# Kernel tuning notes

Hardware: AMD Instinct MI355X
Metric: run time of the kernel (lower is better)

Reference implementation:

```python
import jax, jax.numpy as jnp
import numpy as np


def _conv1x1(x, W, b):
    # x: [B, Cin, H, W]; W: [Cout, Cin]; b: [Cout] -- 1x1 conv == channel matmul
    return jnp.einsum('oc,bchw->bohw', W, x) + b[None, :, None, None]


def setup_inputs() -> dict:
    key = jax.random.key(0)
    ks = jax.random.split(key, 9)
    B, C, H, W = 8, 64, 64, 64
    x = jax.random.normal(ks[0], (B, C, H, W), dtype=jnp.float32)
    y = jax.random.normal(ks[1], (B, C, H, W), dtype=jnp.float32)
    scale = 1.0 / np.sqrt(C)
    Wq = jax.random.normal(ks[2], (C, C), dtype=jnp.float32) * scale
    bq = jax.random.normal(ks[3], (C,), dtype=jnp.float32) * 0.01
    Wk = jax.random.normal(ks[4], (C, C), dtype=jnp.float32) * scale
    bk = jax.random.normal(ks[5], (C,), dtype=jnp.float32) * 0.01
    Wv = jax.random.normal(ks[6], (C, C), dtype=jnp.float32) * scale
    bv = jax.random.normal(ks[7], (C,), dtype=jnp.float32) * 0.01
    # torch inits gamma to 0; use small nonzero value so output/grads are non-trivial
    gamma = jax.random.normal(ks[8], (1,), dtype=jnp.float32) * 0.1
    return {"x": x, "y": y, "Wq": Wq, "bq": bq, "Wk": Wk, "bk": bk,
            "Wv": Wv, "bv": bv, "gamma": gamma}


def reference(x, y, Wq, bq, Wk, bk, Wv, bv, gamma):
    B, C, H, W = x.shape
    N = H * W
    q = _conv1x1(x, Wq, bq)  # [B, C, H, W]
    k = _conv1x1(y, Wk, bk)
    v = _conv1x1(y, Wv, bv)
    # Faithful to torch: raw .view(B, -1, C) memory reinterpretation (NOT a transpose)
    qf = q.reshape(B, N, C)   # reinterprets [B,C,H,W] buffer as [B, N, C]
    kf = k.reshape(B, C, N)
    vf = v.reshape(B, C, N)
    att = jnp.einsum('bnc,bcm->bnm', qf, kf)          # [B, N, N], unscaled
    att = jax.nn.softmax(att, axis=-1)
    out = jnp.einsum('bcj,bij->bci', vf, att)         # bmm(v, att^T) -> [B, C, N]
    out = out.reshape(B, C, H, W)
    return gamma[0] * out + x
```

## Files before the change

kernel.cpp:

```cpp
#include <hip/hip_runtime.h>
#include <math.h>

#define Bb 8
#define Cc 64
#define Nn 4096
#define LOG2E 1.4426950408889634f
#define DEFER_TH 8.0f

typedef __attribute__((ext_vector_type(8))) short bf16x8;
typedef __attribute__((ext_vector_type(4))) float f32x4;
typedef __attribute__((ext_vector_type(4))) int   i32x4;

#define MFMA(a,b,c) __builtin_amdgcn_mfma_f32_16x16x32_bf16((a),(b),(c),0,0,0)

#if __has_builtin(__builtin_amdgcn_exp2f)
#define EXP2F(x) __builtin_amdgcn_exp2f(x)
#else
#define EXP2F(x) exp2f(x)
#endif

__device__ __forceinline__ unsigned short f2bf(float f){
    unsigned uu = __float_as_uint(f);
    return (unsigned short)((uu + 0x7FFFu + ((uu>>16)&1u)) >> 16);
}
__device__ __forceinline__ float bfres(float f, unsigned short h){
    return f - __uint_as_float(((unsigned)h)<<16);
}
__device__ __forceinline__ int swzaddr(int row, int slot){
    int h = (row ^ (row>>3)) & 7;
    return row*128 + (((slot ^ h)&7)<<4);
}

__global__ __launch_bounds__(256) void precompute_q(
    const float* __restrict__ x, const float* __restrict__ Wq,
    const float* __restrict__ bq, unsigned short* __restrict__ wsq)
{
    __shared__ __align__(16) unsigned char XHI[16384];
    __shared__ __align__(16) unsigned char XLO[16384];
    const int tid = threadIdx.x;
    const int l   = tid & 63;
    const int w   = tid >> 6;
    const int l15 = l & 15;
    const int u   = l >> 4;
    const int b   = blockIdx.x & 7;
    const int pt  = blockIdx.x >> 3;
    const int p0  = pt*128;

    bf16x8 whiA[2], wloA[2];
    #pragma unroll
    for (int kc=0; kc<2; ++kc){
        const float* wr = Wq + (16*w + l15)*64 + kc*32 + u*8;
        const float4 f0 = *(const float4*)(wr);
        const float4 f1 = *(const float4*)(wr + 4);
        const float vv[8] = {f0.x,f0.y,f0.z,f0.w,f1.x,f1.y,f1.z,f1.w};
        bf16x8 hi, lo;
        #pragma unroll
        for (int i=0;i<8;++i){
            const unsigned short h = f2bf(vv[i]);
            hi[i] = (short)h;
            lo[i] = (short)f2bf(bfres(vv[i], h));
        }
        whiA[kc]=hi; wloA[kc]=lo;
    }
    {
        const int cx0 = (tid & 31)*2;
        const int pq  = (tid >> 5)*16;
        const float* xr0 = x + ((size_t)b*64 + cx0)*4096 + p0 + pq;
        const float* xr1 = xr0 + 4096;
        #pragma unroll
        for (int q4=0; q4<4; ++q4){
            const float4 a = *(const float4*)(xr0 + q4*4);
            const float4 c = *(const float4*)(xr1 + q4*4);
            const float av[4]={a.x,a.y,a.z,a.w}, cv[4]={c.x,c.y,c.z,c.w};
            #pragma unroll
            for (int k=0;k<4;++k){
                const int p = pq + q4*4 + k;
                const unsigned short h0=f2bf(av[k]), h1=f2bf(cv[k]);
                const unsigned short l0=f2bf(bfres(av[k],h0));
                const unsigned short l1=f2bf(bfres(cv[k],h1));
                const int ad = swzaddr(p, cx0>>3) + (cx0&7)*2;
                *(unsigned int*)(XHI + ad) = (unsigned)h0 | ((unsigned)h1<<16);
                *(unsigned int*)(XLO + ad) = (unsigned)l0 | ((unsigned)l1<<16);
            }
        }
    }
    __syncthreads();

    f32x4 D[8];
    #pragma unroll
    for (int nb=0;nb<8;++nb) D[nb]=(f32x4){0.f,0.f,0.f,0.f};
    #pragma unroll
    for (int nb=0;nb<8;++nb){
        #pragma unroll
        for (int kc=0;kc<2;++kc){
            const int ad = swzaddr(16*nb + l15, kc*4 + u);
            const bf16x8 xh = *(const bf16x8*)(XHI + ad);
            const bf16x8 xl = *(const bf16x8*)(XLO + ad);
            D[nb] = MFMA(whiA[kc], xh, D[nb]);
            D[nb] = MFMA(whiA[kc], xl, D[nb]);
            D[nb] = MFMA(wloA[kc], xh, D[nb]);
        }
    }
    float bq4[4];
    #pragma unroll
    for (int r=0;r<4;++r) bq4[r] = bq[16*w + u*4 + r];
    #pragma unroll
    for (int nb=0;nb<8;++nb){
        #pragma unroll
        for (int r=0;r<4;++r){
            const int c = 16*w + u*4 + r;
            const int p = p0 + 16*nb + l15;
            wsq[((size_t)b*64 + c)*4096 + p] = f2bf(D[nb][r] + bq4[r]);
        }
    }
}

__global__ __launch_bounds__(256,2) void fused_attn2(
    const float* __restrict__ x, const float* __restrict__ y,
    const float* __restrict__ Wk, const unsigned short* __restrict__ wsq,
    const float* __restrict__ Wv, const float* __restrict__ bv,
    const float* __restrict__ gammap, float* __restrict__ out)
{
    __shared__ __align__(16) unsigned char QW [8192];
    __shared__ __align__(16) unsigned char PT [8192];
    __shared__ __align__(16) unsigned char WKT[8192];
    __shared__ __align__(16) unsigned char YN [2][8192];
    __shared__ __align__(16) unsigned char YT [2][8192];

    const int tid = threadIdx.x;
    const int l   = tid & 63;
    const int w   = tid >> 6;
    const int l15 = l & 15;
    const int u   = l >> 4;
    const int b   = blockIdx.x & 7;
    const int blk = blockIdx.x >> 3;
    const int p0  = blk*64;

    const float* __restrict__ yb = y + (size_t)b*Cc*Nn;

    const int sci = tid >> 2;
    const int sj0 = (tid & 3) * 16;

    float4 pf0, pf1, pf2, pf3;
    {
        const float* yr = yb + (size_t)sci*Nn + sj0;
        pf0 = *(const float4*)(yr);
        pf1 = *(const float4*)(yr + 4);
        pf2 = *(const float4*)(yr + 8);
        pf3 = *(const float4*)(yr + 12);
    }

    {
        const int c   = tid >> 2;
        const int ci0 = (tid & 3)*16;
        const float* wr = Wk + c*64 + ci0;
        #pragma unroll
        for (int q4=0; q4<4; ++q4){
            const float4 f = *(const float4*)(wr + q4*4);
            const float fv[4] = {f.x,f.y,f.z,f.w};
            #pragma unroll
            for (int k=0;k<4;++k){
                const int ci = ci0 + q4*4 + k;
                *(unsigned short*)(WKT + swzaddr(ci, c>>3) + (c&7)*2) = f2bf(fv[k]);
            }
        }
    }
    bf16x8 qA[2];
    {
        const unsigned short* qchan = wsq + ((size_t)b*64 + blk)*4096;
        #pragma unroll
        for (int kc=0;kc<2;++kc)
            qA[kc] = *(const bf16x8*)(qchan + 64*(16*w + l15) + kc*32 + u*8);
    }
    __syncthreads();

    {
        f32x4 D2[4];
        #pragma unroll
        for (int nb=0;nb<4;++nb){
            f32x4 d = (f32x4){0.f,0.f,0.f,0.f};
            d = MFMA(qA[0], *(const bf16x8*)(WKT + swzaddr(16*nb + l15, u)),     d);
            d = MFMA(qA[1], *(const bf16x8*)(WKT + swzaddr(16*nb + l15, 4 + u)), d);
            D2[nb] = d;
        }
        #pragma unroll
        for (int nb=0;nb<4;++nb){
            #pragma unroll
            for (int r=0;r<4;++r){
                const int t  = 16*w + u*4 + r;
                const int ci = 16*nb + l15;
                *(unsigned short*)(QW + swzaddr(t, 2*nb + (l15>>3)) + (l15&7)*2)
                    = f2bf(D2[nb][r] * LOG2E);
            }
        }
    }
    bf16x8 qwA[2];
    qwA[0] = *(const bf16x8*)(QW + swzaddr(16*w + l15, u));
    qwA[1] = *(const bf16x8*)(QW + swzaddr(16*w + l15, 4 + u));

    int rd[4][2];
    #pragma unroll
    for (int nb=0;nb<4;++nb){
        rd[nb][0] = swzaddr(16*nb + l15, u);
        rd[nb][1] = swzaddr(16*nb + l15, 4 + u);
    }
    const int paA0 = swzaddr(16*w + l15, u);
    const int paA1 = swzaddr(16*w + l15, 4 + u);
    int pw[4][4];
    #pragma unroll
    for (int r=0;r<4;++r)
        #pragma unroll
        for (int nb=0;nb<4;++nb)
            pw[r][nb] = swzaddr(16*w + u*4 + r, 2*nb + (l15>>3)) + (l15&7)*2;

    auto stage_write = [&](float4 a0, float4 a1, float4 a2, float4 a3, int buf){
        const float v[16] = {a0.x,a0.y,a0.z,a0.w, a1.x,a1.y,a1.z,a1.w,
                             a2.x,a2.y,a2.z,a2.w, a3.x,a3.y,a3.z,a3.w};
        unsigned short e[16];
        #pragma unroll
        for (int k=0;k<16;++k) e[k] = f2bf(v[k]);
        i32x4 pk0, pk1;
        pk0.x = (int)((unsigned)e[0]  | ((unsigned)e[1]<<16));
        pk0.y = (int)((unsigned)e[2]  | ((unsigned)e[3]<<16));
        pk0.z = (int)((unsigned)e[4]  | ((unsigned)e[5]<<16));
        pk0.w = (int)((unsigned)e[6]  | ((unsigned)e[7]<<16));
        pk1.x = (int)((unsigned)e[8]  | ((unsigned)e[9]<<16));
        pk1.y = (int)((unsigned)e[10] | ((unsigned)e[11]<<16));
        pk1.z = (int)((unsigned)e[12] | ((unsigned)e[13]<<16));
        pk1.w = (int)((unsigned)e[14] | ((unsigned)e[15]<<16));
        *(i32x4*)(YN[buf] + swzaddr(sci, (sj0>>3)))     = pk0;
        *(i32x4*)(YN[buf] + swzaddr(sci, (sj0>>3) + 1)) = pk1;
        #pragma unroll
        for (int k=0;k<16;++k)
            *(unsigned short*)(YT[buf] + swzaddr(sj0 + k, sci>>3) + (sci&7)*2) = e[k];
    };

    stage_write(pf0, pf1, pf2, pf3, 0);
    __syncthreads();

    f32x4 PY[4];
    #pragma unroll
    for (int nb=0;nb<4;++nb) PY[nb] = (f32x4){0.f,0.f,0.f,0.f};
    float m4[4], l4[4];
    #pragma unroll
    for (int r=0;r<4;++r){ m4[r] = -1.0e30f; l4[r] = 0.f; }

    for (int jt = 0; jt < 64; ++jt){
        const int cur = jt & 1;
        float4 n0,n1,n2,n3;
        if (jt < 63){
            const float* yr = yb + (size_t)sci*Nn + (jt+1)*64 + sj0;
            n0 = *(const float4*)(yr);
            n1 = *(const float4*)(yr + 4);
            n2 = *(const float4*)(yr + 8);
            n3 = *(const float4*)(yr + 12);
        }
        f32x4 S[4];
        #pragma unroll
        for (int nb=0;nb<4;++nb){
            f32x4 s = (f32x4){0.f,0.f,0.f,0.f};
            s = MFMA(qwA[0], *(const bf16x8*)(YT[cur] + rd[nb][0]), s);
            s = MFMA(qwA[1], *(const bf16x8*)(YT[cur] + rd[nb][1]), s);
            S[nb] = s;
        }
        float pm[4];
        #pragma unroll
        for (int r=0;r<4;++r)
            pm[r] = fmaxf(fmaxf(S[0][r],S[1][r]), fmaxf(S[2][r],S[3][r]));
        #pragma unroll
        for (int st=1; st<16; st<<=1){
            #pragma unroll
            for (int r=0;r<4;++r) pm[r] = fmaxf(pm[r], __shfl_xor(pm[r], st));
        }
        bool need = false;
        #pragma unroll
        for (int r=0;r<4;++r) need = need || (pm[r] > m4[r] + DEFER_TH);
        if (__ballot(need)) {
            #pragma unroll
            for (int r=0;r<4;++r){
                const float mn = fmaxf(m4[r], pm[r]);
                const float sc = EXP2F(m4[r] - mn);
                m4[r] = mn;
                l4[r] *= sc;
                #pragma unroll
                for (int nb=0;nb<4;++nb) PY[nb][r] *= sc;
            }
        }
        float rs[4] = {0.f,0.f,0.f,0.f};
        #pragma unroll
        for (int nb=0;nb<4;++nb){
            #pragma unroll
            for (int r=0;r<4;++r){
                const float e = EXP2F(S[nb][r] - m4[r]);
                S[nb][r] = e;
                rs[r] += e;
            }
        }
        #pragma unroll
        for (int st=1; st<16; st<<=1){
            #pragma unroll
            for (int r=0;r<4;++r) rs[r] += __shfl_xor(rs[r], st);
        }
        #pragma unroll
        for (int r=0;r<4;++r) l4[r] += rs[r];

        #pragma unroll
        for (int r=0;r<4;++r)
            #pragma unroll
            for (int nb=0;nb<4;++nb)
                *(unsigned short*)(PT + pw[r][nb]) = f2bf(S[nb][r]);
        {
            const bf16x8 pa0 = *(const bf16x8*)(PT + paA0);
            const bf16x8 pa1 = *(const bf16x8*)(PT + paA1);
            #pragma unroll
            for (int nb=0;nb<4;++nb){
                f32x4 acc = PY[nb];
                acc = MFMA(pa0, *(const bf16x8*)(YN[cur] + rd[nb][0]), acc);
                acc = MFMA(pa1, *(const bf16x8*)(YN[cur] + rd[nb][1]), acc);
                PY[nb] = acc;
            }
        }
        if (jt < 63) stage_write(n0, n1, n2, n3, cur ^ 1);
        __syncthreads();
    }

    float inv[4];
    #pragma unroll
    for (int r=0;r<4;++r) inv[r] = 1.0f / l4[r];
    #pragma unroll
    for (int r=0;r<4;++r)
        #pragma unroll
        for (int nb=0;nb<4;++nb)
            *(unsigned short*)(PT + pw[r][nb]) = f2bf(PY[nb][r] * inv[r]);
    __syncthreads();

    {
        bf16x8 wvA[2];
        #pragma unroll
        for (int kc=0;kc<2;++kc){
            const float* wr = Wv + (16*w + l15)*64 + kc*32 + u*8;
            const float4 f0 = *(const float4*)(wr);
            const float4 f1 = *(const float4*)(wr + 4);
            const float vv[8] = {f0.x,f0.y,f0.z,f0.w,f1.x,f1.y,f1.z,f1.w};
            bf16x8 t;
            #pragma unroll
            for (int i=0;i<8;++i) t[i] = (short)f2bf(vv[i]);
            wvA[kc] = t;
        }
        f32x4 O[4];
        #pragma unroll
        for (int nb=0;nb<4;++nb){
            f32x4 o = (f32x4){0.f,0.f,0.f,0.f};
            o = MFMA(wvA[0], *(const bf16x8*)(PT + rd[nb][0]), o);
            o = MFMA(wvA[1], *(const bf16x8*)(PT + rd[nb][1]), o);
            O[nb] = o;
        }
        const float g = gammap[0];
        #pragma unroll
        for (int r=0;r<4;++r){
            const int cout = 16*w + u*4 + r;
            const float bvc = bv[cout];
            #pragma unroll
            for (int nb=0;nb<4;++nb){
                const int t = 16*nb + l15;
                const size_t oi = ((size_t)b*64 + cout)*4096 + p0 + t;
                out[oi] = g*(O[nb][r] + bvc) + x[oi];
            }
        }
    }
}

extern "C" void kernel_launch(void* const* d_in, const int* in_sizes, int n_in,
                              void* d_out, int out_size, void* d_ws, size_t ws_size,
                              hipStream_t stream) {
    const float* x  = (const float*)d_in[0];
    const float* y  = (const float*)d_in[1];
    const float* Wq = (const float*)d_in[2];
    const float* bq = (const float*)d_in[3];
    const float* Wk = (const float*)d_in[4];
    const float* Wv = (const float*)d_in[6];
    const float* bv = (const float*)d_in[7];
    const float* g  = (const float*)d_in[8];
    float* outp = (float*)d_out;
    unsigned short* wsq = (unsigned short*)d_ws;

    hipLaunchKernelGGL(precompute_q, dim3(256), dim3(256), 0, stream,
                       x, Wq, bq, wsq);
    hipLaunchKernelGGL(fused_attn2, dim3(512), dim3(256), 0, stream,
                       x, y, Wk, wsq, Wv, bv, g, outp);
}
```

Baseline: 221.2 us.

## Rewrite attention kernel with 32x32 MFMA tiles and register-resident P

The fused attention kernel is rewritten around 32x32x16 bf16 MFMA tiles, with 128 queries per block and 256 blocks instead of 512 blocks of 64 queries. Q·Wk folding, the softmax probabilities and the final Wv projection are kept in registers through lane shuffles and packing, so the QW, PT and WKT shared-memory staging buffers are gone. The y tile staging now writes the transposed copy with vectorized 16-byte stores, and bf16 conversion uses a cheaper round-half-up pack. The precompute_q x staging is also restructured into per-thread column loads with vector LDS writes. The trade-offs are higher register pressure (launch bound lowered to 1 block per SM), half as many blocks to fill the GPU, and slightly different rounding.

```diff
diff --git a/kernel.cpp b/kernel.cpp
--- a/kernel.cpp
+++ b/kernel.cpp
@@ -1,22 +1,22 @@
 #include <hip/hip_runtime.h>
 #include <math.h>
 
-#define Bb 8
-#define Cc 64
-#define Nn 4096
 #define LOG2E 1.4426950408889634f
 #define DEFER_TH 8.0f
 
-typedef __attribute__((ext_vector_type(8))) short bf16x8;
-typedef __attribute__((ext_vector_type(4))) float f32x4;
-typedef __attribute__((ext_vector_type(4))) int   i32x4;
-
-#define MFMA(a,b,c) __builtin_amdgcn_mfma_f32_16x16x32_bf16((a),(b),(c),0,0,0)
+typedef __attribute__((ext_vector_type(8)))  short bf16x8;
+typedef __attribute__((ext_vector_type(4)))  short bf16x4;
+typedef __attribute__((ext_vector_type(4)))  float f32x4;
+typedef __attribute__((ext_vector_type(16))) float f32x16;
+typedef __attribute__((ext_vector_type(4)))  int   i32x4;
+
+#define MFMA16(a,b,c) __builtin_amdgcn_mfma_f32_16x16x32_bf16((a),(b),(c),0,0,0)
+#define MFMA32(a,b,c) __builtin_amdgcn_mfma_f32_32x32x16_bf16((a),(b),(c),0,0,0)
 
 #if __has_builtin(__builtin_amdgcn_exp2f)
-#define EXP2F(x) __builtin_amdgcn_exp2f(x)
+#define EXP2F(v) __builtin_amdgcn_exp2f(v)
 #else
-#define EXP2F(x) exp2f(x)
+#define EXP2F(v) exp2f(v)
 #endif
 
 __device__ __forceinline__ unsigned short f2bf(float f){
@@ -26,10 +26,19 @@
 __device__ __forceinline__ float bfres(float f, unsigned short h){
     return f - __uint_as_float(((unsigned)h)<<16);
 }
-__device__ __forceinline__ int swzaddr(int row, int slot){
-    int h = (row ^ (row>>3)) & 7;
-    return row*128 + (((slot ^ h)&7)<<4);
-}
+__device__ __forceinline__ unsigned packrn(float a, float b){
+    unsigned ua = (__float_as_uint(a) + 0x8000u) >> 16;
+    unsigned ub = (__float_as_uint(b) + 0x8000u) & 0xFFFF0000u;
+    return ua | ub;
+}
+__device__ __forceinline__ unsigned packne(float a, float b){
+    return (unsigned)f2bf(a) | ((unsigned)f2bf(b) << 16);
+}
+__device__ __forceinline__ int lds_rc(int row, int slot){
+    int h = (row ^ (row >> 3)) & 7;
+    return (row << 7) + (((slot ^ h) & 7) << 4);
+}
+union U4 { unsigned u[4]; bf16x8 v; i32x4 i; };
 
 __global__ __launch_bounds__(256) void precompute_q(
     const float* __restrict__ x, const float* __restrict__ Wq,
@@ -38,13 +47,12 @@
     __shared__ __align__(16) unsigned char XHI[16384];
     __shared__ __align__(16) unsigned char XLO[16384];
     const int tid = threadIdx.x;
-    const int l   = tid & 63;
+    const int l15 = tid & 15;
+    const int u   = (tid & 63) >> 4;
     const int w   = tid >> 6;
-    const int l15 = l & 15;
-    const int u   = l >> 4;
     const int b   = blockIdx.x & 7;
     const int pt  = blockIdx.x >> 3;
-    const int p0  = pt*128;
+    const int p0  = pt * 128;
 
     bf16x8 whiA[2], wloA[2];
     #pragma unroll
@@ -63,42 +71,43 @@
         whiA[kc]=hi; wloA[kc]=lo;
     }
     {
-        const int cx0 = (tid & 31)*2;
-        const int pq  = (tid >> 5)*16;
-        const float* xr0 = x + ((size_t)b*64 + cx0)*4096 + p0 + pq;
-        const float* xr1 = xr0 + 4096;
-        #pragma unroll
-        for (int q4=0; q4<4; ++q4){
-            const float4 a = *(const float4*)(xr0 + q4*4);
-            const float4 c = *(const float4*)(xr1 + q4*4);
-            const float av[4]={a.x,a.y,a.z,a.w}, cv[4]={c.x,c.y,c.z,c.w};
-            #pragma unroll
-            for (int k=0;k<4;++k){
-                const int p = pq + q4*4 + k;
-                const unsigned short h0=f2bf(av[k]), h1=f2bf(cv[k]);
-                const unsigned short l0=f2bf(bfres(av[k],h0));
-                const unsigned short l1=f2bf(bfres(cv[k],h1));
-                const int ad = swzaddr(p, cx0>>3) + (cx0&7)*2;
-                *(unsigned int*)(XHI + ad) = (unsigned)h0 | ((unsigned)h1<<16);
-                *(unsigned int*)(XLO + ad) = (unsigned)l0 | ((unsigned)l1<<16);
-            }
+        const int p  = tid & 127;
+        const int hf = tid >> 7;
+        const float* xr = x + ((size_t)(b*64 + hf*32))*4096 + p0 + p;
+        float v[32];
+        #pragma unroll
+        for (int k2=0;k2<32;++k2) v[k2] = xr[(size_t)k2*4096];
+        unsigned hiw[16], low[16];
+        #pragma unroll
+        for (int q2=0;q2<16;++q2){
+            const unsigned short h0 = f2bf(v[2*q2]),  h1 = f2bf(v[2*q2+1]);
+            const unsigned short r0 = f2bf(bfres(v[2*q2],h0)), r1 = f2bf(bfres(v[2*q2+1],h1));
+            hiw[q2] = (unsigned)h0 | ((unsigned)h1<<16);
+            low[q2] = (unsigned)r0 | ((unsigned)r1<<16);
+        }
+        #pragma unroll
+        for (int s=0;s<4;++s){
+            i32x4 a = {(int)hiw[4*s],(int)hiw[4*s+1],(int)hiw[4*s+2],(int)hiw[4*s+3]};
+            i32x4 c2= {(int)low[4*s],(int)low[4*s+1],(int)low[4*s+2],(int)low[4*s+3]};
+            *(i32x4*)(XHI + lds_rc(p, hf*4 + s)) = a;
+            *(i32x4*)(XLO + lds_rc(p, hf*4 + s)) = c2;
         }
     }
     __syncthreads();
 
     f32x4 D[8];
     #pragma unroll
-    for (int nb=0;nb<8;++nb) D[nb]=(f32x4){0.f,0.f,0.f,0.f};
+    for (int nb=0;nb<8;++nb) D[nb] = (f32x4){0.f,0.f,0.f,0.f};
     #pragma unroll
     for (int nb=0;nb<8;++nb){
         #pragma unroll
         for (int kc=0;kc<2;++kc){
-            const int ad = swzaddr(16*nb + l15, kc*4 + u);
+            const int ad = lds_rc(16*nb + l15, 4*kc + u);
             const bf16x8 xh = *(const bf16x8*)(XHI + ad);
             const bf16x8 xl = *(const bf16x8*)(XLO + ad);
-            D[nb] = MFMA(whiA[kc], xh, D[nb]);
-            D[nb] = MFMA(whiA[kc], xl, D[nb]);
-            D[nb] = MFMA(wloA[kc], xh, D[nb]);
+            D[nb] = MFMA16(whiA[kc], xh, D[nb]);
+            D[nb] = MFMA16(whiA[kc], xl, D[nb]);
+            D[nb] = MFMA16(wloA[kc], xh, D[nb]);
         }
     }
     float bq4[4];
@@ -107,265 +116,261 @@
     #pragma unroll
     for (int nb=0;nb<8;++nb){
         #pragma unroll
-        for (int r=0;r<4;++r){
-            const int c = 16*w + u*4 + r;
-            const int p = p0 + 16*nb + l15;
-            wsq[((size_t)b*64 + c)*4096 + p] = f2bf(D[nb][r] + bq4[r]);
-        }
-    }
-}
-
-__global__ __launch_bounds__(256,2) void fused_attn2(
+        for (int r=0;r<4;++r)
+            wsq[((size_t)b*64 + 16*w + u*4 + r)*4096 + p0 + 16*nb + l15]
+                = f2bf(D[nb][r] + bq4[r]);
+    }
+}
+
+__global__ __launch_bounds__(256, 1) void fused_attn3(
     const float* __restrict__ x, const float* __restrict__ y,
     const float* __restrict__ Wk, const unsigned short* __restrict__ wsq,
     const float* __restrict__ Wv, const float* __restrict__ bv,
     const float* __restrict__ gammap, float* __restrict__ out)
 {
-    __shared__ __align__(16) unsigned char QW [8192];
-    __shared__ __align__(16) unsigned char PT [8192];
-    __shared__ __align__(16) unsigned char WKT[8192];
-    __shared__ __align__(16) unsigned char YN [2][8192];
-    __shared__ __align__(16) unsigned char YT [2][8192];
+    __shared__ __align__(16) unsigned char YN[2][8192];
+    __shared__ __align__(16) unsigned char YT[2][8192];
 
     const int tid = threadIdx.x;
     const int l   = tid & 63;
     const int w   = tid >> 6;
-    const int l15 = l & 15;
-    const int u   = l >> 4;
+    const int l31 = l & 31;
+    const int g   = l >> 5;
     const int b   = blockIdx.x & 7;
-    const int blk = blockIdx.x >> 3;
-    const int p0  = blk*64;
-
-    const float* __restrict__ yb = y + (size_t)b*Cc*Nn;
-
-    const int sci = tid >> 2;
-    const int sj0 = (tid & 3) * 16;
-
-    float4 pf0, pf1, pf2, pf3;
+    const int pb  = blockIdx.x >> 3;
+    const int n0  = pb * 128;
+
+    const float* __restrict__ yb = y + (size_t)b*64*4096;
+
+    f32x16 QC0, QC1;
+    #pragma unroll
+    for (int i=0;i<16;++i){ QC0[i]=0.f; QC1[i]=0.f; }
     {
-        const float* yr = yb + (size_t)sci*Nn + sj0;
-        pf0 = *(const float4*)(yr);
-        pf1 = *(const float4*)(yr + 4);
-        pf2 = *(const float4*)(yr + 8);
-        pf3 = *(const float4*)(yr + 12);
-    }
-
+        const int ch  = (pb*2) + (w >> 1);
+        const unsigned short* qrow = wsq + ((size_t)b*64 + ch)*4096 + ((w&1)*32 + l31)*64;
+        #pragma unroll
+        for (int kc=0;kc<4;++kc){
+            const bf16x8 qb = *(const bf16x8*)(qrow + 16*kc + g*8);
+            #pragma unroll
+            for (int rowb=0;rowb<2;++rowb){
+                bf16x8 wa;
+                #pragma unroll
+                for (int i=0;i<8;++i)
+                    wa[i] = (short)f2bf(Wk[(16*kc + g*8 + i)*64 + 32*rowb + l31]);
+                if (rowb==0) QC0 = MFMA32(wa, qb, QC0);
+                else         QC1 = MFMA32(wa, qb, QC1);
+            }
+        }
+    }
+    bf16x8 qwB[4];
     {
-        const int c   = tid >> 2;
-        const int ci0 = (tid & 3)*16;
-        const float* wr = Wk + c*64 + ci0;
-        #pragma unroll
-        for (int q4=0; q4<4; ++q4){
-            const float4 f = *(const float4*)(wr + q4*4);
-            const float fv[4] = {f.x,f.y,f.z,f.w};
-            #pragma unroll
-            for (int k=0;k<4;++k){
-                const int ci = ci0 + q4*4 + k;
-                *(unsigned short*)(WKT + swzaddr(ci, c>>3) + (c&7)*2) = f2bf(fv[k]);
-            }
-        }
-    }
-    bf16x8 qA[2];
+        unsigned qp[2][8], qq[2][8];
+        #pragma unroll
+        for (int m=0;m<8;++m){
+            qp[0][m] = packne(QC0[2*m]*LOG2E, QC0[2*m+1]*LOG2E);
+            qp[1][m] = packne(QC1[2*m]*LOG2E, QC1[2*m+1]*LOG2E);
+        }
+        #pragma unroll
+        for (int rb=0;rb<2;++rb)
+            #pragma unroll
+            for (int m=0;m<8;++m) qq[rb][m] = __shfl_xor((int)qp[rb][m], 32);
+        #pragma unroll
+        for (int kc=0;kc<4;++kc){
+            const int rb = kc>>1, h = kc&1;
+            U4 uu;
+            if (g==0){ uu.u[0]=qp[rb][4*h+0]; uu.u[1]=qp[rb][4*h+1];
+                       uu.u[2]=qq[rb][4*h+0]; uu.u[3]=qq[rb][4*h+1]; }
+            else     { uu.u[0]=qq[rb][4*h+2]; uu.u[1]=qq[rb][4*h+3];
+                       uu.u[2]=qp[rb][4*h+2]; uu.u[3]=qp[rb][4*h+3]; }
+            qwB[kc] = uu.v;
+        }
+    }
+
+    const int nci = tid >> 2, njq = tid & 3;
+    const int tj  = tid & 63, tcq = tid >> 6;
+    const int wnat0 = lds_rc(nci, njq*2),     wnat1 = lds_rc(nci, njq*2 + 1);
+    const int wtr0  = lds_rc(tj,  tcq*2),     wtr1  = lds_rc(tj,  tcq*2 + 1);
+    int rS[2][4];
+    #pragma unroll
+    for (int jb=0;jb<2;++jb)
+        #pragma unroll
+        for (int kc=0;kc<4;++kc) rS[jb][kc] = lds_rc(32*jb + l31, 2*kc + g);
+    int rPa[2][4][2];
+    #pragma unroll
+    for (int cib=0;cib<2;++cib)
+        #pragma unroll
+        for (int kcp=0;kcp<4;++kcp){
+            const int jb = kcp>>1, h = kcp&1;
+            rPa[cib][kcp][0] = lds_rc(l31 + 32*cib, 4*jb + 2*h)     + 8*g;
+            rPa[cib][kcp][1] = lds_rc(l31 + 32*cib, 4*jb + 2*h + 1) + 8*g;
+        }
+    const float* gnat = yb + (size_t)nci*4096 + njq*16;
+    const float* gtr  = yb + (size_t)(tcq*16)*4096 + tj;
+
+    f32x16 OC0, OC1;
+    #pragma unroll
+    for (int i=0;i<16;++i){ OC0[i]=0.f; OC1[i]=0.f; }
+    float m = -1.0e30f, lsum = 0.f;
+
     {
-        const unsigned short* qchan = wsq + ((size_t)b*64 + blk)*4096;
-        #pragma unroll
-        for (int kc=0;kc<2;++kc)
-            qA[kc] = *(const bf16x8*)(qchan + 64*(16*w + l15) + kc*32 + u*8);
+        float4 a0 = *(const float4*)(gnat);
+        float4 a1 = *(const float4*)(gnat + 4);
+        float4 a2 = *(const float4*)(gnat + 8);
+        float4 a3 = *(const float4*)(gnat + 12);
+        float tv[16];
+        #pragma unroll
+        for (int k2=0;k2<16;++k2) tv[k2] = gtr[(size_t)k2*4096];
+        const float nvv[16] = {a0.x,a0.y,a0.z,a0.w,a1.x,a1.y,a1.z,a1.w,
+                               a2.x,a2.y,a2.z,a2.w,a3.x,a3.y,a3.z,a3.w};
+        unsigned nk[8], tk[8];
+        #pragma unroll
+        for (int q2=0;q2<8;++q2){ nk[q2]=packrn(nvv[2*q2],nvv[2*q2+1]);
+                                  tk[q2]=packrn(tv[2*q2], tv[2*q2+1]); }
+        i32x4 w0={(int)nk[0],(int)nk[1],(int)nk[2],(int)nk[3]};
+        i32x4 w1={(int)nk[4],(int)nk[5],(int)nk[6],(int)nk[7]};
+        i32x4 w2={(int)tk[0],(int)tk[1],(int)tk[2],(int)tk[3]};
+        i32x4 w3={(int)tk[4],(int)tk[5],(int)tk[6],(int)tk[7]};
+        *(i32x4*)(YN[0] + wnat0) = w0;  *(i32x4*)(YN[0] + wnat1) = w1;
+        *(i32x4*)(YT[0] + wtr0)  = w2;  *(i32x4*)(YT[0] + wtr1)  = w3;
     }
     __syncthreads();
-
-    {
-        f32x4 D2[4];
-        #pragma unroll
-        for (int nb=0;nb<4;++nb){
-            f32x4 d = (f32x4){0.f,0.f,0.f,0.f};
-            d = MFMA(qA[0], *(const bf16x8*)(WKT + swzaddr(16*nb + l15, u)),     d);
-            d = MFMA(qA[1], *(const bf16x8*)(WKT + swzaddr(16*nb + l15, 4 + u)), d);
-            D2[nb] = d;
-        }
-        #pragma unroll
-        for (int nb=0;nb<4;++nb){
-            #pragma unroll
-            for (int r=0;r<4;++r){
-                const int t  = 16*w + u*4 + r;
-                const int ci = 16*nb + l15;
-                *(unsigned short*)(QW + swzaddr(t, 2*nb + (l15>>3)) + (l15&7)*2)
-                    = f2bf(D2[nb][r] * LOG2E);
-            }
-        }
-    }
-    bf16x8 qwA[2];
-    qwA[0] = *(const bf16x8*)(QW + swzaddr(16*w + l15, u));
-    qwA[1] = *(const bf16x8*)(QW + swzaddr(16*w + l15, 4 + u));
-
-    int rd[4][2];
-    #pragma unroll
-    for (int nb=0;nb<4;++nb){
-        rd[nb][0] = swzaddr(16*nb + l15, u);
-        rd[nb][1] = swzaddr(16*nb + l15, 4 + u);
-    }
-    const int paA0 = swzaddr(16*w + l15, u);
-    const int paA1 = swzaddr(16*w + l15, 4 + u);
-    int pw[4][4];
-    #pragma unroll
-    for (int r=0;r<4;++r)
-        #pragma unroll
-        for (int nb=0;nb<4;++nb)
-            pw[r][nb] = swzaddr(16*w + u*4 + r, 2*nb + (l15>>3)) + (l15&7)*2;
-
-    auto stage_write = [&](float4 a0, float4 a1, float4 a2, float4 a3, int buf){
-        const float v[16] = {a0.x,a0.y,a0.z,a0.w, a1.x,a1.y,a1.z,a1.w,
-                             a2.x,a2.y,a2.z,a2.w, a3.x,a3.y,a3.z,a3.w};
-        unsigned short e[16];
-        #pragma unroll
-        for (int k=0;k<16;++k) e[k] = f2bf(v[k]);
-        i32x4 pk0, pk1;
-        pk0.x = (int)((unsigned)e[0]  | ((unsigned)e[1]<<16));
-        pk0.y = (int)((unsigned)e[2]  | ((unsigned)e[3]<<16));
-        pk0.z = (int)((unsigned)e[4]  | ((unsigned)e[5]<<16));
-        pk0.w = (int)((unsigned)e[6]  | ((unsigned)e[7]<<16));
-        pk1.x = (int)((unsigned)e[8]  | ((unsigned)e[9]<<16));
-        pk1.y = (int)((unsigned)e[10] | ((unsigned)e[11]<<16));
-        pk1.z = (int)((unsigned)e[12] | ((unsigned)e[13]<<16));
-        pk1.w = (int)((unsigned)e[14] | ((unsigned)e[15]<<16));
-        *(i32x4*)(YN[buf] + swzaddr(sci, (sj0>>3)))     = pk0;
-        *(i32x4*)(YN[buf] + swzaddr(sci, (sj0>>3) + 1)) = pk1;
-        #pragma unroll
-        for (int k=0;k<16;++k)
-            *(unsigned short*)(YT[buf] + swzaddr(sj0 + k, sci>>3) + (sci&7)*2) = e[k];
-    };
-
-    stage_write(pf0, pf1, pf2, pf3, 0);
-    __syncthreads();
-
-    f32x4 PY[4];
-    #pragma unroll
-    for (int nb=0;nb<4;++nb) PY[nb] = (f32x4){0.f,0.f,0.f,0.f};
-    float m4[4], l4[4];
-    #pragma unroll
-    for (int r=0;r<4;++r){ m4[r] = -1.0e30f; l4[r] = 0.f; }
 
     for (int jt = 0; jt < 64; ++jt){
         const int cur = jt & 1;
-        float4 n0,n1,n2,n3;
-        if (jt < 63){
-            const float* yr = yb + (size_t)sci*Nn + (jt+1)*64 + sj0;
-            n0 = *(const float4*)(yr);
-            n1 = *(const float4*)(yr + 4);
-            n2 = *(const float4*)(yr + 8);
-            n3 = *(const float4*)(yr + 12);
-        }
-        f32x4 S[4];
-        #pragma unroll
-        for (int nb=0;nb<4;++nb){
-            f32x4 s = (f32x4){0.f,0.f,0.f,0.f};
-            s = MFMA(qwA[0], *(const bf16x8*)(YT[cur] + rd[nb][0]), s);
-            s = MFMA(qwA[1], *(const bf16x8*)(YT[cur] + rd[nb][1]), s);
-            S[nb] = s;
-        }
-        float pm[4];
-        #pragma unroll
-        for (int r=0;r<4;++r)
-            pm[r] = fmaxf(fmaxf(S[0][r],S[1][r]), fmaxf(S[2][r],S[3][r]));
-        #pragma unroll
-        for (int st=1; st<16; st<<=1){
-            #pragma unroll
-            for (int r=0;r<4;++r) pm[r] = fmaxf(pm[r], __shfl_xor(pm[r], st));
-        }
-        bool need = false;
-        #pragma unroll
-        for (int r=0;r<4;++r) need = need || (pm[r] > m4[r] + DEFER_TH);
-        if (__ballot(need)) {
-            #pragma unroll
-            for (int r=0;r<4;++r){
-                const float mn = fmaxf(m4[r], pm[r]);
-                const float sc = EXP2F(m4[r] - mn);
-                m4[r] = mn;
-                l4[r] *= sc;
+        const bool pf = (jt < 63);
+        float4 a0,a1,a2,a3; float tv[16];
+        if (pf){
+            const float* gn = gnat + (jt+1)*64;
+            a0 = *(const float4*)(gn);     a1 = *(const float4*)(gn + 4);
+            a2 = *(const float4*)(gn + 8); a3 = *(const float4*)(gn + 12);
+            const float* gt = gtr + (jt+1)*64;
+            #pragma unroll
+            for (int k2=0;k2<16;++k2) tv[k2] = gt[(size_t)k2*4096];
+        }
+        f32x16 SC0, SC1;
+        #pragma unroll
+        for (int i=0;i<16;++i){ SC0[i]=0.f; SC1[i]=0.f; }
+        #pragma unroll
+        for (int kc=0;kc<4;++kc){
+            SC0 = MFMA32(*(const bf16x8*)(YT[cur] + rS[0][kc]), qwB[kc], SC0);
+            SC1 = MFMA32(*(const bf16x8*)(YT[cur] + rS[1][kc]), qwB[kc], SC1);
+        }
+        float mx[16];
+        #pragma unroll
+        for (int i=0;i<16;++i) mx[i] = fmaxf(SC0[i], SC1[i]);
+        #pragma unroll
+        for (int s=8;s>=1;s>>=1)
+            #pragma unroll
+            for (int i=0;i<s;++i) mx[i] = fmaxf(mx[i], mx[i+s]);
+        float pm = fmaxf(mx[0], __shfl_xor(mx[0], 32));
+        if (__ballot(pm > m + DEFER_TH)) {
+            const float mn = fmaxf(m, pm);
+            const float sc = EXP2F(m - mn);
+            m = mn; lsum *= sc;
+            #pragma unroll
+            for (int i=0;i<16;++i){ OC0[i]*=sc; OC1[i]*=sc; }
+        }
+        float p0f[16], p1f[16];
+        #pragma unroll
+        for (int i=0;i<16;++i){ p0f[i]=EXP2F(SC0[i]-m); p1f[i]=EXP2F(SC1[i]-m); }
+        float sm[16];
+        #pragma unroll
+        for (int i=0;i<16;++i) sm[i] = p0f[i] + p1f[i];
+        #pragma unroll
+        for (int s=8;s>=1;s>>=1)
+            #pragma unroll
+            for (int i=0;i<s;++i) sm[i] += sm[i+s];
+        lsum += sm[0] + __shfl_xor(sm[0], 32);
+        unsigned pk0[8], pk1[8];
+        #pragma unroll
+        for (int q2=0;q2<8;++q2){ pk0[q2]=packrn(p0f[2*q2],p0f[2*q2+1]);
+                                  pk1[q2]=packrn(p1f[2*q2],p1f[2*q2+1]); }
+        #pragma unroll
+        for (int kcp=0;kcp<4;++kcp){
+            const int h = kcp&1;
+            U4 pb4;
+            if (kcp<2){ pb4.u[0]=pk0[4*h+0]; pb4.u[1]=pk0[4*h+1];
+                        pb4.u[2]=pk0[4*h+2]; pb4.u[3]=pk0[4*h+3]; }
+            else      { pb4.u[0]=pk1[4*h+0]; pb4.u[1]=pk1[4*h+1];
+                        pb4.u[2]=pk1[4*h+2]; pb4.u[3]=pk1[4*h+3]; }
+            {
+                bf16x4 y0 = *(const bf16x4*)(YN[cur] + rPa[0][kcp][0]);
+                bf16x4 y1 = *(const bf16x4*)(YN[cur] + rPa[0][kcp][1]);
+                bf16x8 ya; 
                 #pragma unroll
-                for (int nb=0;nb<4;++nb) PY[nb][r] *= sc;
+                for (int i=0;i<4;++i){ ya[i]=y0[i]; ya[4+i]=y1[i]; }
+                OC0 = MFMA32(ya, pb4.v, OC0);
             }
-        }
-        float rs[4] = {0.f,0.f,0.f,0.f};
-        #pragma unroll
-        for (int nb=0;nb<4;++nb){
-            #pragma unroll
-            for (int r=0;r<4;++r){
-                const float e = EXP2F(S[nb][r] - m4[r]);
-                S[nb][r] = e;
-                rs[r] += e;
+            {
+                bf16x4 y0 = *(const bf16x4*)(YN[cur] + rPa[1][kcp][0]);
+                bf16x4 y1 = *(const bf16x4*)(YN[cur] + rPa[1][kcp][1]);
+                bf16x8 ya;
+                #pragma unroll
+                for (int i=0;i<4;++i){ ya[i]=y0[i]; ya[4+i]=y1[i]; }
+                OC1 = MFMA32(ya, pb4.v, OC1);
             }
         }
-        #pragma unroll
-        for (int st=1; st<16; st<<=1){
-            #pragma unroll
-            for (int r=0;r<4;++r) rs[r] += __shfl_xor(rs[r], st);
-        }
-        #pragma unroll
-        for (int r=0;r<4;++r) l4[r] += rs[r];
-
-        #pragma unroll
-        for (int r=0;r<4;++r)
-            #pragma unroll
-            for (int nb=0;nb<4;++nb)
-                *(unsigned short*)(PT + pw[r][nb]) = f2bf(S[nb][r]);
-        {
-            const bf16x8 pa0 = *(const bf16x8*)(PT + paA0);
-            const bf16x8 pa1 = *(const bf16x8*)(PT + paA1);
-            #pragma unroll
-            for (int nb=0;nb<4;++nb){
-                f32x4 acc = PY[nb];
-                acc = MFMA(pa0, *(const bf16x8*)(YN[cur] + rd[nb][0]), acc);
-                acc = MFMA(pa1, *(const bf16x8*)(YN[cur] + rd[nb][1]), acc);
-                PY[nb] = acc;
-            }
-        }
-        if (jt < 63) stage_write(n0, n1, n2, n3, cur ^ 1);
+        if (pf){
+            const float nvv[16] = {a0.x,a0.y,a0.z,a0.w,a1.x,a1.y,a1.z,a1.w,
+                                   a2.x,a2.y,a2.z,a2.w,a3.x,a3.y,a3.z,a3.w};
+            unsigned nk[8], tk[8];
+            #pragma unroll
+            for (int q2=0;q2<8;++q2){ nk[q2]=packrn(nvv[2*q2],nvv[2*q2+1]);
+                                      tk[q2]=packrn(tv[2*q2], tv[2*q2+1]); }
+            const int nxt = cur ^ 1;
+            i32x4 w0={(int)nk[0],(int)nk[1],(int)nk[2],(int)nk[3]};
+            i32x4 w1={(int)nk[4],(int)nk[5],(int)nk[6],(int)nk[7]};
+            i32x4 w2={(int)tk[0],(int)tk[1],(int)tk[2],(int)tk[3]};
+            i32x4 w3={(int)tk[4],(int)tk[5],(int)tk[6],(int)tk[7]};
+            *(i32x4*)(YN[nxt] + wnat0) = w0;  *(i32x4*)(YN[nxt] + wnat1) = w1;
+            *(i32x4*)(YT[nxt] + wtr0)  = w2;  *(i32x4*)(YT[nxt] + wtr1)  = w3;
+        }
         __syncthreads();
     }
 
-    float inv[4];
-    #pragma unroll
-    for (int r=0;r<4;++r) inv[r] = 1.0f / l4[r];
-    #pragma unroll
-    for (int r=0;r<4;++r)
-        #pragma unroll
-        for (int nb=0;nb<4;++nb)
-            *(unsigned short*)(PT + pw[r][nb]) = f2bf(PY[nb][r] * inv[r]);
-    __syncthreads();
-
-    {
-        bf16x8 wvA[2];
-        #pragma unroll
-        for (int kc=0;kc<2;++kc){
-            const float* wr = Wv + (16*w + l15)*64 + kc*32 + u*8;
+    const float inv = 1.0f / lsum;
+    unsigned ok0[8], ok1[8];
+    #pragma unroll
+    for (int q2=0;q2<8;++q2){
+        ok0[q2] = packne(OC0[2*q2]*inv, OC0[2*q2+1]*inv);
+        ok1[q2] = packne(OC1[2*q2]*inv, OC1[2*q2+1]*inv);
+    }
+    f32x16 ZC0, ZC1;
+    #pragma unroll
+    for (int i=0;i<16;++i){ ZC0[i]=0.f; ZC1[i]=0.f; }
+    #pragma unroll
+    for (int kcz=0;kcz<4;++kcz){
+        const int cib = kcz>>1, h = kcz&1;
+        U4 pb4;
+        if (cib==0){ pb4.u[0]=ok0[4*h+0]; pb4.u[1]=ok0[4*h+1];
+                     pb4.u[2]=ok0[4*h+2]; pb4.u[3]=ok0[4*h+3]; }
+        else       { pb4.u[0]=ok1[4*h+0]; pb4.u[1]=ok1[4*h+1];
+                     pb4.u[2]=ok1[4*h+2]; pb4.u[3]=ok1[4*h+3]; }
+        const int j0c = 32*cib + 16*h + 4*g;
+        #pragma unroll
+        for (int rowb=0;rowb<2;++rowb){
+            const float* wr = Wv + (size_t)(32*rowb + l31)*64 + j0c;
             const float4 f0 = *(const float4*)(wr);
-            const float4 f1 = *(const float4*)(wr + 4);
-            const float vv[8] = {f0.x,f0.y,f0.z,f0.w,f1.x,f1.y,f1.z,f1.w};
-            bf16x8 t;
-            #pragma unroll
-            for (int i=0;i<8;++i) t[i] = (short)f2bf(vv[i]);
-            wvA[kc] = t;
-        }
-        f32x4 O[4];
-        #pragma unroll
-        for (int nb=0;nb<4;++nb){
-            f32x4 o = (f32x4){0.f,0.f,0.f,0.f};
-            o = MFMA(wvA[0], *(const bf16x8*)(PT + rd[nb][0]), o);
-            o = MFMA(wvA[1], *(const bf16x8*)(PT + rd[nb][1]), o);
-            O[nb] = o;
-        }
-        const float g = gammap[0];
-        #pragma unroll
-        for (int r=0;r<4;++r){
-            const int cout = 16*w + u*4 + r;
-            const float bvc = bv[cout];
-            #pragma unroll
-            for (int nb=0;nb<4;++nb){
-                const int t = 16*nb + l15;
-                const size_t oi = ((size_t)b*64 + cout)*4096 + p0 + t;
-                out[oi] = g*(O[nb][r] + bvc) + x[oi];
-            }
+            const float4 f1 = *(const float4*)(wr + 8);
+            bf16x8 wa;
+            wa[0]=(short)f2bf(f0.x); wa[1]=(short)f2bf(f0.y);
+            wa[2]=(short)f2bf(f0.z); wa[3]=(short)f2bf(f0.w);
+            wa[4]=(short)f2bf(f1.x); wa[5]=(short)f2bf(f1.y);
+            wa[6]=(short)f2bf(f1.z); wa[7]=(short)f2bf(f1.w);
+            if (rowb==0) ZC0 = MFMA32(wa, pb4.v, ZC0);
+            else         ZC1 = MFMA32(wa, pb4.v, ZC1);
+        }
+    }
+    const float gm = gammap[0];
+    const int n = n0 + 32*w + l31;
+    #pragma unroll
+    for (int rowb=0;rowb<2;++rowb){
+        #pragma unroll
+        for (int reg=0;reg<16;++reg){
+            const int c = 32*rowb + (reg&3) + 8*(reg>>2) + 4*g;
+            const size_t oi = ((size_t)b*64 + c)*4096 + n;
+            const float zv = (rowb==0) ? ZC0[reg] : ZC1[reg];
+            out[oi] = gm*(zv + bv[c]) + x[oi];
         }
     }
 }
@@ -384,8 +389,7 @@
     float* outp = (float*)d_out;
     unsigned short* wsq = (unsigned short*)d_ws;
 
-    hipLaunchKernelGGL(precompute_q, dim3(256), dim3(256), 0, stream,
-                       x, Wq, bq, wsq);
-    hipLaunchKernelGGL(fused_attn2, dim3(512), dim3(256), 0, stream,
+    hipLaunchKernelGGL(precompute_q, dim3(256), dim3(256), 0, stream, x, Wq, bq, wsq);
+    hipLaunchKernelGGL(fused_attn3, dim3(256), dim3(256), 0, stream,
                        x, y, Wk, wsq, Wv, bv, g, outp);
 }
```

New measurement: 180.6 us. 1.22x faster.
